# Kernel tuning notes

Hardware: AMD Instinct MI355X
Metric: run time of the kernel (lower is better)

The kernel has to match this reference:

```python
import jax, jax.numpy as jnp
import numpy as np

EMBED_DIM = 512
N_HEADS = 16
HEAD_DIM = EMBED_DIM // N_HEADS  # 32


def setup_inputs() -> dict:
    key0 = jax.random.key(0)
    ks = jax.random.split(key0, 8)
    B, S, D = 4, 2048, EMBED_DIM
    inp = {
        "key": jax.random.normal(ks[0], (B, S, D), dtype=jnp.float32),
        "query": jax.random.normal(ks[1], (B, S, D), dtype=jnp.float32),
        "value": jax.random.normal(ks[2], (B, S, D), dtype=jnp.float32),
        # per-head projection weights (nn.Linear: y = x @ W.T), no bias
        "Wq": jax.random.normal(ks[3], (HEAD_DIM, HEAD_DIM), dtype=jnp.float32) * 0.1,
        "Wk": jax.random.normal(ks[4], (HEAD_DIM, HEAD_DIM), dtype=jnp.float32) * 0.1,
        "Wv": jax.random.normal(ks[5], (HEAD_DIM, HEAD_DIM), dtype=jnp.float32) * 0.1,
        # output projection with bias
        "Wo": jax.random.normal(ks[6], (EMBED_DIM, EMBED_DIM), dtype=jnp.float32) * 0.05,
        "bo": jax.random.normal(ks[7], (EMBED_DIM,), dtype=jnp.float32) * 0.01,
    }
    return inp


def reference(key, query, value, Wq, Wk, Wv, Wo, bo):
    B, S, D = key.shape
    Sq = query.shape[1]
    H, dh = N_HEADS, HEAD_DIM
    # reshape to [B, S, H, dh] then per-head linear (x @ W.T)
    k = jnp.einsum('bshd,ed->bhse', key.reshape(B, S, H, dh), Wk)
    q = jnp.einsum('bshd,ed->bhse', query.reshape(B, Sq, H, dh), Wq)
    v = jnp.einsum('bshd,ed->bhse', value.reshape(B, S, H, dh), Wv)
    # naive attention: full [B,H,Sq,S] scores
    scores = jnp.einsum('bhqd,bhkd->bhqk', q, k) / jnp.sqrt(jnp.float32(dh))
    attn = jax.nn.softmax(scores, axis=-1)
    ctx = jnp.einsum('bhqk,bhkd->bhqd', attn, v)  # [B,H,Sq,dh]
    concat = ctx.transpose(0, 2, 1, 3).reshape(B, Sq, H * dh)
    return concat @ Wo.T + bo
```

## Files before the change

kernel.cpp:

```cpp
#include <hip/hip_runtime.h>
#include <hip/hip_bf16.h>


typedef __attribute__((ext_vector_type(8))) short bf16x8;
typedef __attribute__((ext_vector_type(4))) float f32x4;

#define MFMA16(a, b, c) __builtin_amdgcn_mfma_f32_16x16x32_bf16(a, b, c, 0, 0, 0)

static __device__ __forceinline__ unsigned short f2bf(float f) {
  __bf16 h = (__bf16)f;
  union { __bf16 h; unsigned short u; } c; c.h = h; return c.u;
}
static __device__ __forceinline__ float bf2f(unsigned short u) {
  union { unsigned u; float f; } c; c.u = ((unsigned)u) << 16; return c.f;
}

static __device__ __forceinline__ void gld_lds16(const ushort* g, ushort* l) {
  __builtin_amdgcn_global_load_lds(
      (const __attribute__((address_space(1))) unsigned int*)g,
      (__attribute__((address_space(3))) unsigned int*)l, 16, 0, 0);
}

static __device__ __forceinline__ void load8_split(const float* p, bf16x8& hi, bf16x8& lo) {
  float4 a = *(const float4*)p;
  float4 b = *(const float4*)(p + 4);
  float v[8] = {a.x, a.y, a.z, a.w, b.x, b.y, b.z, b.w};
  #pragma unroll
  for (int j = 0; j < 8; ++j) {
    unsigned short h = f2bf(v[j]);
    hi[j] = (short)h;
    lo[j] = (short)f2bf(v[j] - bf2f(h));
  }
}

__global__ __launch_bounds__(256) void wcvt_kernel(const float* __restrict__ Wo,
                                                   ushort* __restrict__ Wob) {
  int i = (blockIdx.x * 256 + threadIdx.x) * 4;
  float4 v = *(const float4*)&Wo[i];
  ushort4 o;
  o.x = f2bf(v.x); o.y = f2bf(v.y); o.z = f2bf(v.z); o.w = f2bf(v.w);
  *(ushort4*)&Wob[i] = o;
}

__global__ __launch_bounds__(256) void proj_kernel(
    const float* __restrict__ key, const float* __restrict__ query,
    const float* __restrict__ value,
    const float* __restrict__ Wq, const float* __restrict__ Wk,
    const float* __restrict__ Wv,
    ushort* __restrict__ Qp, ushort* __restrict__ Kp, ushort* __restrict__ Vt) {
  const int tid = threadIdx.x;
  const int l = tid & 63, wid = tid >> 6;
  const int lr = l & 15, lc = l >> 4;
  const int task = blockIdx.x * 4 + wid;
  const int h = task & 15;
  const int st = (task >> 4) & 127;
  const int b = task >> 11;
  const int bh = b * 16 + h;
  const size_t xoff = ((size_t)b * 2048 + st * 16 + lr) * 512 + h * 32 + lc * 8;
  const float ALPHA = 0.2550354039f;

  #pragma unroll
  for (int t = 0; t < 3; ++t) {
    const float* x = (t == 0) ? query : (t == 1) ? key : value;
    const float* W = (t == 0) ? Wq : (t == 1) ? Wk : Wv;
    bf16x8 xh, xl;
    load8_split(x + xoff, xh, xl);
    #pragma unroll
    for (int eh = 0; eh < 2; ++eh) {
      bf16x8 wh, wl;
      load8_split(W + (size_t)(eh * 16 + lr) * 32 + lc * 8, wh, wl);
      f32x4 acc = {0.f, 0.f, 0.f, 0.f};
      acc = MFMA16(xh, wh, acc);
      acc = MFMA16(xh, wl, acc);
      acc = MFMA16(xl, wh, acc);
      if (t == 0) {
        #pragma unroll
        for (int r = 0; r < 4; ++r)
          Qp[((size_t)bh * 2048 + st * 16 + lc * 4 + r) * 32 + eh * 16 + lr] =
              f2bf(acc[r] * ALPHA);
      } else if (t == 1) {
        #pragma unroll
        for (int r = 0; r < 4; ++r)
          Kp[((size_t)bh * 2048 + st * 16 + lc * 4 + r) * 32 + eh * 16 + lr] = f2bf(acc[r]);
      } else {
        ushort4 pk;
        pk.x = f2bf(acc[0]); pk.y = f2bf(acc[1]);
        pk.z = f2bf(acc[2]); pk.w = f2bf(acc[3]);
        *(ushort4*)&Vt[((size_t)bh * 32 + eh * 16 + lr) * 2048 + st * 16 + lc * 4] = pk;
      }
    }
  }
}

__global__ __launch_bounds__(256) void attn_kernel(
    const ushort* __restrict__ Qp, const ushort* __restrict__ Kp,
    const ushort* __restrict__ Vt, ushort* __restrict__ Cb) {
  __shared__ ushort plds[4][16][68];
  __shared__ ushort kbuf[3][2048];
  __shared__ ushort vbuf[3][2048];
  const int tid = threadIdx.x;
  const int l = tid & 63, w = tid >> 6;
  const int lr = l & 15, lc = l >> 4;
  const int xcd = blockIdx.x & 7, idx = blockIdx.x >> 3;
  const int bh = xcd * 8 + (idx >> 4);
  const int qblk = idx & 15;
  const int b = bh >> 4, h = bh & 15;
  const int q0 = qblk * 128 + w * 32;

  const ushort* Qb = Qp + (size_t)bh * 2048 * 32;
  const ushort* Kb = Kp + (size_t)bh * 2048 * 32;
  const ushort* Vb = Vt + (size_t)bh * 32 * 2048;

  const int sig = tid ^ ((tid >> 3) & 7);
  const ushort* kg_src = Kb + (size_t)sig * 8;
  const ushort* vg_src = Vb + (size_t)(tid >> 3) * 2048 +
                         (((tid & 7) ^ ((tid >> 3) & 7)) * 8);

  int koff[4];
  #pragma unroll
  for (int kg = 0; kg < 4; ++kg) {
    int v = (kg * 16 + lr) * 4 + lc;
    v ^= (v >> 3) & 7;
    koff[kg] = v * 8;
  }
  int voff[2][2];
  #pragma unroll
  for (int kc = 0; kc < 2; ++kc)
    #pragma unroll
    for (int eh = 0; eh < 2; ++eh) {
      int v = (eh * 16 + lr) * 8 + kc * 4 + lc;
      v ^= (v >> 3) & 7;
      voff[kc][eh] = v * 8;
    }

  bf16x8 qf[2];
  qf[0] = *(const bf16x8*)&Qb[(size_t)(q0 + lr) * 32 + lc * 8];
  qf[1] = *(const bf16x8*)&Qb[(size_t)(q0 + 16 + lr) * 32 + lc * 8];

  bf16x8 ones;
  #pragma unroll
  for (int j = 0; j < 8; ++j) ones[j] = (short)0x3F80;

  f32x4 octx[2][2] = {};
  f32x4 dacc[2] = {};
  const f32x4 zero = {0.f, 0.f, 0.f, 0.f};

  gld_lds16(kg_src, &kbuf[0][tid * 8]);
  gld_lds16(vg_src, &vbuf[0][tid * 8]);
  gld_lds16(kg_src + (size_t)64 * 32, &kbuf[1][tid * 8]);
  gld_lds16(vg_src + 64, &vbuf[1][tid * 8]);
  asm volatile("s_waitcnt vmcnt(2)" ::: "memory");
  __builtin_amdgcn_s_barrier();

  int cur = 0, nx2 = 2;
  for (int kt = 0; kt < 32; ++kt) {
    if (kt < 30) {
      const int k0n = (kt + 2) * 64;
      gld_lds16(kg_src + (size_t)k0n * 32, &kbuf[nx2][tid * 8]);
      gld_lds16(vg_src + k0n, &vbuf[nx2][tid * 8]);
    }

    const ushort* kb = kbuf[cur];
    const ushort* vb = vbuf[cur];
    bf16x8 kf[4];
    #pragma unroll
    for (int kg = 0; kg < 4; ++kg)
      kf[kg] = *(const bf16x8*)&kb[koff[kg]];
    bf16x8 vf[2][2];
    #pragma unroll
    for (int kc = 0; kc < 2; ++kc)
      #pragma unroll
      for (int eh = 0; eh < 2; ++eh)
        vf[kc][eh] = *(const bf16x8*)&vb[voff[kc][eh]];

    #pragma unroll
    for (int qi = 0; qi < 2; ++qi) {
      f32x4 sc[4];
      #pragma unroll
      for (int kg = 0; kg < 4; ++kg)
        sc[kg] = MFMA16(kf[kg], qf[qi], zero);
      #pragma unroll
      for (int kg = 0; kg < 4; ++kg) {
        float p0 = __builtin_amdgcn_exp2f(sc[kg][0]);
        float p1 = __builtin_amdgcn_exp2f(sc[kg][1]);
        float p2 = __builtin_amdgcn_exp2f(sc[kg][2]);
        float p3 = __builtin_amdgcn_exp2f(sc[kg][3]);
        ushort4 pk;
        pk.x = f2bf(p0); pk.y = f2bf(p1); pk.z = f2bf(p2); pk.w = f2bf(p3);
        *(ushort4*)&plds[w][lr][kg * 16 + lc * 4] = pk;
      }
      #pragma unroll
      for (int kc = 0; kc < 2; ++kc) {
        union { ushort4 q[2]; bf16x8 v; } u;
        u.q[0] = *(const ushort4*)&plds[w][lr][kc * 32 + lc * 8];
        u.q[1] = *(const ushort4*)&plds[w][lr][kc * 32 + lc * 8 + 4];
        #pragma unroll
        for (int eh = 0; eh < 2; ++eh)
          octx[qi][eh] = MFMA16(u.v, vf[kc][eh], octx[qi][eh]);
        dacc[qi] = MFMA16(u.v, ones, dacc[qi]);
      }
    }

    if (kt < 30) {
      asm volatile("s_waitcnt vmcnt(2)" ::: "memory");
    } else {
      asm volatile("s_waitcnt vmcnt(0)" ::: "memory");
    }
    __builtin_amdgcn_s_barrier();
    cur = (cur == 2) ? 0 : cur + 1;
    nx2 = (nx2 == 2) ? 0 : nx2 + 1;
  }

  #pragma unroll
  for (int qi = 0; qi < 2; ++qi) {
    float inv[4];
    #pragma unroll
    for (int r = 0; r < 4; ++r)
      inv[r] = 1.0f / dacc[qi][r];
    #pragma unroll
    for (int eh = 0; eh < 2; ++eh)
      #pragma unroll
      for (int r = 0; r < 4; ++r) {
        float v = octx[qi][eh][r] * inv[r];
        Cb[((size_t)b * 2048 + q0 + qi * 16 + lc * 4 + r) * 512 + h * 32 + eh * 16 + lr] =
            f2bf(v);
      }
  }
}

__global__ __launch_bounds__(256) void oproj_kernel(
    const ushort* __restrict__ Cb, const ushort* __restrict__ Wob,
    const float* __restrict__ bo, float* __restrict__ out) {
  const int tid = threadIdx.x;
  const int l = tid & 63, w = tid >> 6;
  const int lr = l & 15, lc = l >> 4;
  const int qt = blockIdx.x >> 1;
  const int nt = blockIdx.x & 1;
  const int r0 = qt * 64;
  const int n0 = nt * 256 + w * 64;

  f32x4 acc[4][4] = {};
  for (int kk = 0; kk < 16; ++kk) {
    const int k0 = kk * 32;
    bf16x8 af[4], bf[4];
    #pragma unroll
    for (int i = 0; i < 4; ++i)
      af[i] = *(const bf16x8*)&Cb[(size_t)(r0 + i * 16 + lr) * 512 + k0 + lc * 8];
    #pragma unroll
    for (int j = 0; j < 4; ++j)
      bf[j] = *(const bf16x8*)&Wob[(size_t)(n0 + j * 16 + lr) * 512 + k0 + lc * 8];
    #pragma unroll
    for (int i = 0; i < 4; ++i)
      #pragma unroll
      for (int j = 0; j < 4; ++j)
        acc[i][j] = MFMA16(af[i], bf[j], acc[i][j]);
  }
  #pragma unroll
  for (int j = 0; j < 4; ++j) {
    float bias = bo[n0 + j * 16 + lr];
    #pragma unroll
    for (int i = 0; i < 4; ++i)
      #pragma unroll
      for (int r = 0; r < 4; ++r)
        out[(size_t)(r0 + i * 16 + lc * 4 + r) * 512 + n0 + j * 16 + lr] =
            acc[i][j][r] + bias;
  }
}

extern "C" void kernel_launch(void* const* d_in, const int* in_sizes, int n_in,
                              void* d_out, int out_size, void* d_ws, size_t ws_size,
                              hipStream_t stream) {
  (void)in_sizes; (void)n_in; (void)out_size; (void)ws_size;
  const float* key   = (const float*)d_in[0];
  const float* query = (const float*)d_in[1];
  const float* value = (const float*)d_in[2];
  const float* Wq    = (const float*)d_in[3];
  const float* Wk    = (const float*)d_in[4];
  const float* Wv    = (const float*)d_in[5];
  const float* Wo    = (const float*)d_in[6];
  const float* bo    = (const float*)d_in[7];
  float* out = (float*)d_out;

  const size_t NT = (size_t)4 * 16 * 2048 * 32;
  ushort* ws  = (ushort*)d_ws;
  ushort* Qp  = ws;
  ushort* Kp  = Qp + NT;
  ushort* Vt  = Kp + NT;
  ushort* Cb  = Vt + NT;
  ushort* Wob = Cb + NT;

  hipLaunchKernelGGL(wcvt_kernel, dim3(256), dim3(256), 0, stream, Wo, Wob);
  hipLaunchKernelGGL(proj_kernel, dim3(2048), dim3(256), 0, stream,
                     key, query, value, Wq, Wk, Wv, Qp, Kp, Vt);
  hipLaunchKernelGGL(attn_kernel, dim3(1024), dim3(256), 0, stream, Qp, Kp, Vt, Cb);
  hipLaunchKernelGGL(oproj_kernel, dim3(256), dim3(256), 0, stream, Cb, Wob, bo, out);
}
```

Before: 108.3 us.

## Load V fragments directly from global and retile output projection for more blocks

```diff
diff --git a/kernel.cpp b/kernel.cpp
--- a/kernel.cpp
+++ b/kernel.cpp
@@ -97,7 +97,6 @@
     const ushort* __restrict__ Vt, ushort* __restrict__ Cb) {
   __shared__ ushort plds[4][16][68];
   __shared__ ushort kbuf[3][2048];
-  __shared__ ushort vbuf[3][2048];
   const int tid = threadIdx.x;
   const int l = tid & 63, w = tid >> 6;
   const int lr = l & 15, lc = l >> 4;
@@ -113,8 +112,6 @@
 
   const int sig = tid ^ ((tid >> 3) & 7);
   const ushort* kg_src = Kb + (size_t)sig * 8;
-  const ushort* vg_src = Vb + (size_t)(tid >> 3) * 2048 +
-                         (((tid & 7) ^ ((tid >> 3) & 7)) * 8);
 
   int koff[4];
   #pragma unroll
@@ -123,15 +120,8 @@
     v ^= (v >> 3) & 7;
     koff[kg] = v * 8;
   }
-  int voff[2][2];
-  #pragma unroll
-  for (int kc = 0; kc < 2; ++kc)
-    #pragma unroll
-    for (int eh = 0; eh < 2; ++eh) {
-      int v = (eh * 16 + lr) * 8 + kc * 4 + lc;
-      v ^= (v >> 3) & 7;
-      voff[kc][eh] = v * 8;
-    }
+  const ushort* vrow0 = Vb + (size_t)lr * 2048 + lc * 8;
+  const ushort* vrow1 = Vb + (size_t)(16 + lr) * 2048 + lc * 8;
 
   bf16x8 qf[2];
   qf[0] = *(const bf16x8*)&Qb[(size_t)(q0 + lr) * 32 + lc * 8];
@@ -146,32 +136,27 @@
   const f32x4 zero = {0.f, 0.f, 0.f, 0.f};
 
   gld_lds16(kg_src, &kbuf[0][tid * 8]);
-  gld_lds16(vg_src, &vbuf[0][tid * 8]);
   gld_lds16(kg_src + (size_t)64 * 32, &kbuf[1][tid * 8]);
-  gld_lds16(vg_src + 64, &vbuf[1][tid * 8]);
-  asm volatile("s_waitcnt vmcnt(2)" ::: "memory");
+  asm volatile("s_waitcnt vmcnt(1)" ::: "memory");
   __builtin_amdgcn_s_barrier();
 
   int cur = 0, nx2 = 2;
   for (int kt = 0; kt < 32; ++kt) {
-    if (kt < 30) {
-      const int k0n = (kt + 2) * 64;
-      gld_lds16(kg_src + (size_t)k0n * 32, &kbuf[nx2][tid * 8]);
-      gld_lds16(vg_src + k0n, &vbuf[nx2][tid * 8]);
-    }
+    const int k0 = kt * 64;
+    if (kt < 30)
+      gld_lds16(kg_src + (size_t)(k0 + 128) * 32, &kbuf[nx2][tid * 8]);
 
     const ushort* kb = kbuf[cur];
-    const ushort* vb = vbuf[cur];
     bf16x8 kf[4];
     #pragma unroll
     for (int kg = 0; kg < 4; ++kg)
       kf[kg] = *(const bf16x8*)&kb[koff[kg]];
     bf16x8 vf[2][2];
     #pragma unroll
-    for (int kc = 0; kc < 2; ++kc)
-      #pragma unroll
-      for (int eh = 0; eh < 2; ++eh)
-        vf[kc][eh] = *(const bf16x8*)&vb[voff[kc][eh]];
+    for (int kc = 0; kc < 2; ++kc) {
+      vf[kc][0] = *(const bf16x8*)&vrow0[k0 + kc * 32];
+      vf[kc][1] = *(const bf16x8*)&vrow1[k0 + kc * 32];
+    }
 
     #pragma unroll
     for (int qi = 0; qi < 2; ++qi) {
@@ -202,7 +187,7 @@
     }
 
     if (kt < 30) {
-      asm volatile("s_waitcnt vmcnt(2)" ::: "memory");
+      asm volatile("s_waitcnt vmcnt(1)" ::: "memory");
     } else {
       asm volatile("s_waitcnt vmcnt(0)" ::: "memory");
     }
@@ -234,36 +219,25 @@
   const int tid = threadIdx.x;
   const int l = tid & 63, w = tid >> 6;
   const int lr = l & 15, lc = l >> 4;
-  const int qt = blockIdx.x >> 1;
-  const int nt = blockIdx.x & 1;
-  const int r0 = qt * 64;
-  const int n0 = nt * 256 + w * 64;
-
-  f32x4 acc[4][4] = {};
+  const int r0 = (blockIdx.x >> 3) * 64 + w * 16;
+  const int n0 = (blockIdx.x & 7) * 64;
+
+  f32x4 acc[4] = {};
   for (int kk = 0; kk < 16; ++kk) {
     const int k0 = kk * 32;
-    bf16x8 af[4], bf[4];
-    #pragma unroll
-    for (int i = 0; i < 4; ++i)
-      af[i] = *(const bf16x8*)&Cb[(size_t)(r0 + i * 16 + lr) * 512 + k0 + lc * 8];
-    #pragma unroll
-    for (int j = 0; j < 4; ++j)
-      bf[j] = *(const bf16x8*)&Wob[(size_t)(n0 + j * 16 + lr) * 512 + k0 + lc * 8];
-    #pragma unroll
-    for (int i = 0; i < 4; ++i)
-      #pragma unroll
-      for (int j = 0; j < 4; ++j)
-        acc[i][j] = MFMA16(af[i], bf[j], acc[i][j]);
+    bf16x8 af = *(const bf16x8*)&Cb[(size_t)(r0 + lr) * 512 + k0 + lc * 8];
+    #pragma unroll
+    for (int j = 0; j < 4; ++j) {
+      bf16x8 bf = *(const bf16x8*)&Wob[(size_t)(n0 + j * 16 + lr) * 512 + k0 + lc * 8];
+      acc[j] = MFMA16(af, bf, acc[j]);
+    }
   }
   #pragma unroll
   for (int j = 0; j < 4; ++j) {
     float bias = bo[n0 + j * 16 + lr];
     #pragma unroll
-    for (int i = 0; i < 4; ++i)
-      #pragma unroll
-      for (int r = 0; r < 4; ++r)
-        out[(size_t)(r0 + i * 16 + lc * 4 + r) * 512 + n0 + j * 16 + lr] =
-            acc[i][j][r] + bias;
+    for (int r = 0; r < 4; ++r)
+      out[(size_t)(r0 + lc * 4 + r) * 512 + n0 + j * 16 + lr] = acc[j][r] + bias;
   }
 }
 
@@ -293,5 +267,5 @@
   hipLaunchKernelGGL(proj_kernel, dim3(2048), dim3(256), 0, stream,
                      key, query, value, Wq, Wk, Wv, Qp, Kp, Vt);
   hipLaunchKernelGGL(attn_kernel, dim3(1024), dim3(256), 0, stream, Qp, Kp, Vt, Cb);
-  hipLaunchKernelGGL(oproj_kernel, dim3(256), dim3(256), 0, stream, Cb, Wob, bo, out);
-}
+  hipLaunchKernelGGL(oproj_kernel, dim3(1024), dim3(256), 0, stream, Cb, Wob, bo, out);
+}
```

Result: slower. 144.3 us (+33.2%).
